# Optimization experiments

Hardware: AMD Instinct MI355X
Metric: run time of the kernel (lower is better)

## Reference

```python
import jax, jax.numpy as jnp
import numpy as np
from jax import lax

B, C, H, W = 4, 256, 64, 64
NH, DK, DV = 8, 32, 32
KER, PAD = 3, 1


def conv1x1(x, w, b=None):
    # x: [B,C,H,W], w: [O,C] (1x1 conv kernel), b: [O] or None
    y = jnp.einsum('bchw,oc->bohw', x, w)
    if b is not None:
        y = y + b[None, :, None, None]
    return y


def unfold(x, k, pad):
    # F.unfold equivalent: [B,C,H,W] -> [B, C*k*k, H, W] (channel-major patch order)
    return lax.conv_general_dilated_patches(x, (k, k), (1, 1), [(pad, pad), (pad, pad)])


def local_attention(q, k, v, kernel, pad, n_head):
    # per-head local windowed attention over a kernel x kernel neighborhood
    b, c, h, w = q.shape
    d = c // n_head
    kk = kernel * kernel
    qh = q.reshape(b, n_head, d, h, w)
    kpat = unfold(k, kernel, pad).reshape(b, n_head, d, kk, h, w)
    vpat = unfold(v, kernel, pad).reshape(b, n_head, d, kk, h, w)
    scale = 1.0 / np.sqrt(float(d)).astype(np.float32)
    logits = jnp.einsum('bhdxy,bhdkxy->bhkxy', qh, kpat) * scale
    attn = jax.nn.softmax(logits, axis=2)
    out = jnp.einsum('bhkxy,bhdkxy->bhdxy', attn, vpat)
    return out.reshape(b, c, h, w)


def layernorm2d(x, g, b, eps=1e-6):
    mu = jnp.mean(x, axis=1, keepdims=True)
    var = jnp.mean((x - mu) ** 2, axis=1, keepdims=True)
    return (x - mu) / jnp.sqrt(var + eps) * g[None, :, None, None] + b[None, :, None, None]


def batchnorm2d(x, g, b, eps=1e-5):
    mu = jnp.mean(x, axis=(0, 2, 3), keepdims=True)
    var = jnp.mean((x - mu) ** 2, axis=(0, 2, 3), keepdims=True)
    return (x - mu) / jnp.sqrt(var + eps) * g[None, :, None, None] + b[None, :, None, None]


def mha(xq, xkv, wq, wk, wv, wfc, g, bias, kernel, pad):
    residual = xq
    q = conv1x1(xq, wq)
    k = conv1x1(xkv, wk)
    v = conv1x1(xkv, wv)
    o = local_attention(q, k, v, kernel, pad, NH)
    o = conv1x1(o, wfc) + residual
    return layernorm2d(o, g, bias)


def ffn(x, w1, b1, w2, b2, g, bias):
    residual = x
    y = conv1x1(jax.nn.relu(conv1x1(x, w1, b1)), w2, b2)
    y = batchnorm2d(y, g, bias)
    return y + residual


def setup_inputs() -> dict:
    key = jax.random.key(0)
    ks = jax.random.split(key, 16)
    s = 0.05
    d = {
        'input1': jax.random.normal(ks[0], (B, C, H, W), jnp.float32),
        'input2': jax.random.normal(ks[1], (B, C, H, W), jnp.float32),
        'slf_wq': jax.random.normal(ks[2], (NH * DK, C), jnp.float32) * s,
        'slf_wk': jax.random.normal(ks[3], (NH * DK, C), jnp.float32) * s,
        'slf_wv': jax.random.normal(ks[4], (NH * DV, C), jnp.float32) * s,
        'slf_fc': jax.random.normal(ks[5], (C, NH * DV), jnp.float32) * s,
        'slf_g': jnp.ones((C,), jnp.float32),
        'slf_b': jnp.zeros((C,), jnp.float32),
        'crs_wq': jax.random.normal(ks[6], (NH * DK, C), jnp.float32) * s,
        'crs_wk': jax.random.normal(ks[7], (NH * DK, C), jnp.float32) * s,
        'crs_wv': jax.random.normal(ks[8], (NH * DV, C), jnp.float32) * s,
        'crs_fc': jax.random.normal(ks[9], (C, NH * DV), jnp.float32) * s,
        'crs_g': jnp.ones((C,), jnp.float32),
        'crs_b': jnp.zeros((C,), jnp.float32),
        'ffn_w1': jax.random.normal(ks[10], (C, C), jnp.float32) * s,
        'ffn_b1': jnp.zeros((C,), jnp.float32),
        'ffn_w2': jax.random.normal(ks[11], (C, C), jnp.float32) * s,
        'ffn_b2': jnp.zeros((C,), jnp.float32),
        'ffn_bn_g': jnp.ones((C,), jnp.float32),
        'ffn_bn_b': jnp.zeros((C,), jnp.float32),
        'kernel': KER,
        'pad': PAD,
    }
    return d


def reference(input1, input2, slf_wq, slf_wk, slf_wv, slf_fc, slf_g, slf_b,
              crs_wq, crs_wk, crs_wv, crs_fc, crs_g, crs_b,
              ffn_w1, ffn_b1, ffn_w2, ffn_b2, ffn_bn_g, ffn_bn_b, kernel, pad):
    slf1 = mha(input1, input1, slf_wq, slf_wk, slf_wv, slf_fc, slf_g, slf_b, kernel, pad)
    slf2 = mha(input2, input2, slf_wq, slf_wk, slf_wv, slf_fc, slf_g, slf_b, kernel, pad)
    crs1 = mha(slf1, slf2, crs_wq, crs_wk, crs_wv, crs_fc, crs_g, crs_b, kernel, pad)
    crs2 = mha(slf2, slf1, crs_wq, crs_wk, crs_wv, crs_fc, crs_g, crs_b, kernel, pad)
    out1 = ffn(crs1, ffn_w1, ffn_b1, ffn_w2, ffn_b2, ffn_bn_g, ffn_bn_b)
    out2 = ffn(crs2, ffn_w1, ffn_b1, ffn_w2, ffn_b2, ffn_bn_g, ffn_bn_b)
    return (out1, out2)
```

## Files before the change

kernel.cpp:

```cpp
#include <hip/hip_runtime.h>
#include <stdint.h>

using u16 = unsigned short;
typedef __bf16 bf16x8 __attribute__((ext_vector_type(8)));
typedef __bf16 bf16x2 __attribute__((ext_vector_type(2)));
typedef float f32x4 __attribute__((ext_vector_type(4)));

#define NPIX 16384
#define CDIM 256

__device__ __forceinline__ float b2f(u16 u) {
  union { unsigned i; float f; } c; c.i = ((unsigned)u) << 16; return c.f;
}
__device__ __forceinline__ u16 f2b(float x) {
  union { __bf16 h; u16 u; } c; c.h = (__bf16)x; return c.u;
}
__device__ __forceinline__ unsigned pack2(float a, float b) {
  union { bf16x2 v; unsigned u; } c; c.v[0] = (__bf16)a; c.v[1] = (__bf16)b; return c.u;
}
__device__ __forceinline__ void unpack8(uint4 w, float* f) {
  f[0] = b2f((u16)(w.x & 0xffffu)); f[1] = b2f((u16)(w.x >> 16));
  f[2] = b2f((u16)(w.y & 0xffffu)); f[3] = b2f((u16)(w.y >> 16));
  f[4] = b2f((u16)(w.z & 0xffffu)); f[5] = b2f((u16)(w.z >> 16));
  f[6] = b2f((u16)(w.w & 0xffffu)); f[7] = b2f((u16)(w.w >> 16));
}

__device__ __forceinline__ void async16(u16* l, const u16* g) {
  __builtin_amdgcn_global_load_lds((const __attribute__((address_space(1))) void*)g,
                                   (__attribute__((address_space(3))) void*)l, 16, 0, 0);
}

template <int NI, int NT>
__device__ __forceinline__ void stage_swz(u16* lds, const u16* src, int tid) {
#pragma unroll
  for (int i = 0; i < NI; ++i) {
    const int idx = i * NT + tid;
    const int row = idx >> 3;
    const int c8 = (idx & 7) ^ (row & 7);
    async16(lds + idx * 8, src + (size_t)row * 256 + c8 * 8);
  }
}

__global__ void prep(const float* __restrict__ x1, const float* __restrict__ x2,
                     u16* __restrict__ X1, u16* __restrict__ X2,
                     const float* s0, const float* s1, const float* s2,
                     const float* s3, const float* s4, const float* s5,
                     const float* s6, const float* s7, const float* s8,
                     const float* s9, u16* __restrict__ wdst,
                     float* __restrict__ stats) {
  const int t = threadIdx.x;
  const int yy = blockIdx.y;
  if (yy >= 32) {
    const int m = yy - 32;
    if (m == 0 && blockIdx.x == 0) {
      ((float4*)stats)[t] = float4{0.f, 0.f, 0.f, 0.f};
    }
    const float* s;
    switch (m) {
      case 0: s = s0; break; case 1: s = s1; break; case 2: s = s2; break;
      case 3: s = s3; break; case 4: s = s4; break; case 5: s = s5; break;
      case 6: s = s6; break; case 7: s = s7; break; case 8: s = s8; break;
      default: s = s9; break;
    }
    const int i = (blockIdx.x * 256 + t) * 4;
    float4 v = *(const float4*)(s + i);
    uint2 o;
    o.x = pack2(v.x, v.y);
    o.y = pack2(v.z, v.w);
    *(uint2*)(wdst + (size_t)m * 65536 + i) = o;
    return;
  }
  __shared__ u16 tile[64][65];
  const int z = yy >> 2;
  const float* x = (z < 4) ? x1 : x2;
  u16* X = (z < 4) ? X1 : X2;
  const int b = z & 3, c0 = (yy & 3) * 64, hw0 = blockIdx.x * 64;
  {
    const int hw_l = t & 63, cb = t >> 6;
#pragma unroll
    for (int i = 0; i < 16; ++i) {
      const int c_l = cb * 16 + i;
      tile[c_l][hw_l] = f2b(x[((size_t)(b * 256 + c0 + c_l)) * 4096 + hw0 + hw_l]);
    }
  }
  __syncthreads();
  {
    const int c_l = t & 63, hb = t >> 6;
#pragma unroll
    for (int i = 0; i < 16; ++i) {
      const int hw_l = hb * 16 + i;
      X[((size_t)(b * 4096 + hw0 + hw_l)) * 256 + c0 + c_l] = tile[c_l][hw_l];
    }
  }
}

struct PG { const u16* X[6]; const u16* W[3]; u16* D[6];
            const float* bias; float* st[2]; };

template <int NG, int HAS_BIAS, int RELU, int DO_STATS>
__global__ void gemm128(PG a) {
  __shared__ u16 As[2][8192];
  __shared__ u16 Bs[2][8192];
  const int tid = threadIdx.x;
  const int wave = tid >> 6, lane = tid & 63;
  const int p0 = blockIdx.x * 128;
  const int g = (NG == 3) ? (blockIdx.y >> 1) : 0;
  const int o0 = (NG == 3) ? ((blockIdx.y & 1) * 128) : (blockIdx.y * 128);
  const int z = blockIdx.z;
  const u16* X = a.X[z * NG + g];
  const u16* W = a.W[g];
  u16* D = a.D[z * NG + g];
  const int wr = wave & 1, wc = wave >> 1;
  const int l15 = lane & 15, l4 = lane >> 4;
  const int sw = l15 & 7;
  f32x4 acc[4][4] = {};

  const u16* Xp = X + (size_t)p0 * 256;
  const u16* Wp = W + (size_t)o0 * 256;
  stage_swz<4, 256>(As[0], Xp, tid);
  stage_swz<4, 256>(Bs[0], Wp, tid);
  __syncthreads();

  for (int kt = 0; kt < 4; ++kt) {
    const int cur = kt & 1;
    if (kt < 3) {
      stage_swz<4, 256>(As[cur ^ 1], Xp + (kt + 1) * 64, tid);
      stage_swz<4, 256>(Bs[cur ^ 1], Wp + (kt + 1) * 64, tid);
    }
    const u16* ab = As[cur];
    const u16* bb = Bs[cur];
#pragma unroll
    for (int kk = 0; kk < 2; ++kk) {
      const int cs = ((kk * 4 + l4) ^ sw) * 8;
      bf16x8 af[4], bfr[4];
#pragma unroll
      for (int mi = 0; mi < 4; ++mi)
        af[mi] = *(const bf16x8*)&ab[(wr * 64 + mi * 16 + l15) * 64 + cs];
#pragma unroll
      for (int ni = 0; ni < 4; ++ni)
        bfr[ni] = *(const bf16x8*)&bb[(wc * 64 + ni * 16 + l15) * 64 + cs];
#pragma unroll
      for (int mi = 0; mi < 4; ++mi)
#pragma unroll
        for (int ni = 0; ni < 4; ++ni)
          acc[mi][ni] = __builtin_amdgcn_mfma_f32_16x16x32_bf16(af[mi], bfr[ni],
                                                                acc[mi][ni], 0, 0, 0);
    }
    __syncthreads();
  }

#pragma unroll
  for (int ni = 0; ni < 4; ++ni) {
    const int o = o0 + wc * 64 + ni * 16 + l15;
    float bvv = 0.f;
    if (HAS_BIAS) bvv = a.bias[o];
    float s = 0.f, s2 = 0.f;
#pragma unroll
    for (int mi = 0; mi < 4; ++mi) {
#pragma unroll
      for (int r = 0; r < 4; ++r) {
        const int p = p0 + wr * 64 + mi * 16 + l4 * 4 + r;
        float v = acc[mi][ni][r] + bvv;
        if (RELU) v = fmaxf(v, 0.f);
        const u16 hv = f2b(v);
        D[(size_t)p * 256 + o] = hv;
        if (DO_STATS) { const float vr = b2f(hv); s += vr; s2 += vr * vr; }
      }
    }
    if (DO_STATS) {
      s += __shfl_xor(s, 16); s2 += __shfl_xor(s2, 16);
      s += __shfl_xor(s, 32); s2 += __shfl_xor(s2, 32);
      if (l4 == 0) {
        atomicAdd(&a.st[z][o], s);
        atomicAdd(&a.st[z][256 + o], s2);
      }
    }
  }
}

struct Pfc { const u16* X[2]; const u16* res[2]; u16* dst[2];
             const u16* W; const float* g; const float* b; };

__global__ __launch_bounds__(512) void gemm_fc_ln(Pfc a) {
  __shared__ u16 As[2][8192];
  __shared__ u16 Bs[2][16384];
  __shared__ float red[2][128][4];
  const int tid = threadIdx.x;
  const int wave = tid >> 6, lane = tid & 63;
  const int wr = wave & 1, wc = wave >> 1;
  const int l15 = lane & 15, l4 = lane >> 4;
  const int sw = l15 & 7;
  const int p0 = blockIdx.x * 128;
  const int z = blockIdx.y;
  const u16* X = a.X[z];
  const u16* res = a.res[z];
  u16* dst = a.dst[z];
  f32x4 acc[4][4] = {};

  const u16* Xp = X + (size_t)p0 * 256;
  stage_swz<2, 512>(As[0], Xp, tid);
  stage_swz<4, 512>(Bs[0], a.W, tid);
  __syncthreads();

  for (int kt = 0; kt < 4; ++kt) {
    const int cur = kt & 1;
    if (kt < 3) {
      stage_swz<2, 512>(As[cur ^ 1], Xp + (kt + 1) * 64, tid);
      stage_swz<4, 512>(Bs[cur ^ 1], a.W + (kt + 1) * 64, tid);
    }
    const u16* ab = As[cur];
    const u16* bb = Bs[cur];
#pragma unroll
    for (int kk = 0; kk < 2; ++kk) {
      const int cs = ((kk * 4 + l4) ^ sw) * 8;
      bf16x8 af[4], bfr[4];
#pragma unroll
      for (int mi = 0; mi < 4; ++mi)
        af[mi] = *(const bf16x8*)&ab[(wr * 64 + mi * 16 + l15) * 64 + cs];
#pragma unroll
      for (int ni = 0; ni < 4; ++ni)
        bfr[ni] = *(const bf16x8*)&bb[(wc * 64 + ni * 16 + l15) * 64 + cs];
#pragma unroll
      for (int mi = 0; mi < 4; ++mi)
#pragma unroll
        for (int ni = 0; ni < 4; ++ni)
          acc[mi][ni] = __builtin_amdgcn_mfma_f32_16x16x32_bf16(af[mi], bfr[ni],
                                                                acc[mi][ni], 0, 0, 0);
    }
    __syncthreads();
  }

#pragma unroll
  for (int mi = 0; mi < 4; ++mi) {
#pragma unroll
    for (int r = 0; r < 4; ++r) {
      const int pl = wr * 64 + mi * 16 + l4 * 4 + r;
      const int p = p0 + pl;
      float s = 0.f, s2 = 0.f;
#pragma unroll
      for (int ni = 0; ni < 4; ++ni) {
        const int o = wc * 64 + ni * 16 + l15;
        float vv = acc[mi][ni][r] + b2f(res[(size_t)p * 256 + o]);
        acc[mi][ni][r] = vv;
        s += vv; s2 += vv * vv;
      }
#pragma unroll
      for (int m = 1; m < 16; m <<= 1) {
        s += __shfl_xor(s, m); s2 += __shfl_xor(s2, m);
      }
      if (l15 == 0) { red[0][pl][wc] = s; red[1][pl][wc] = s2; }
    }
  }
  __syncthreads();

  float gv[4], bv[4];
#pragma unroll
  for (int ni = 0; ni < 4; ++ni) {
    const int o = wc * 64 + ni * 16 + l15;
    gv[ni] = a.g[o]; bv[ni] = a.b[o];
  }
#pragma unroll
  for (int mi = 0; mi < 4; ++mi) {
#pragma unroll
    for (int r = 0; r < 4; ++r) {
      const int pl = wr * 64 + mi * 16 + l4 * 4 + r;
      const float st = red[0][pl][0] + red[0][pl][1] + red[0][pl][2] + red[0][pl][3];
      const float s2t = red[1][pl][0] + red[1][pl][1] + red[1][pl][2] + red[1][pl][3];
      const float mu = st * (1.f / 256.f);
      const float var = s2t * (1.f / 256.f) - mu * mu;
      const float inv = rsqrtf(var + 1e-6f);
      const int p = p0 + pl;
#pragma unroll
      for (int ni = 0; ni < 4; ++ni) {
        const int o = wc * 64 + ni * 16 + l15;
        dst[(size_t)p * 256 + o] = f2b((acc[mi][ni][r] - mu) * inv * gv[ni] + bv[ni]);
      }
    }
  }
}

struct Pat { const u16* Q[2]; const u16* K[2]; const u16* V[2]; u16* O[2]; };

__global__ void attn_kernel(Pat a) {
  const int s = blockIdx.y;
  const u16* __restrict__ Q = a.Q[s];
  const u16* __restrict__ K = a.K[s];
  const u16* __restrict__ V = a.V[s];
  u16* O = a.O[s];
  const int t = blockIdx.x * 256 + threadIdx.x;
  const int p = t >> 3, h = t & 7;
  const int y = (p >> 6) & 63, x = p & 63;
  const size_t base = (size_t)p * 256 + h * 32;

  float q[32];
  {
    const uint4* qp = (const uint4*)(Q + base);
#pragma unroll
    for (int i = 0; i < 4; ++i) { uint4 w = qp[i]; unpack8(w, q + i * 8); }
  }
  float lg[9];
  float mx = -1e30f;
#pragma unroll
  for (int j = 0; j < 9; ++j) {
    const int dy = j / 3 - 1, dx = j % 3 - 1;
    const int ny = y + dy, nx = x + dx;
    float l = 0.f;
    if ((unsigned)ny < 64u && (unsigned)nx < 64u) {
      const uint4* kp = (const uint4*)(K + base + (ptrdiff_t)(dy * 64 + dx) * 256);
      float acc = 0.f;
#pragma unroll
      for (int i = 0; i < 4; ++i) {
        float kf[8]; unpack8(kp[i], kf);
#pragma unroll
        for (int d = 0; d < 8; ++d) acc += q[i * 8 + d] * kf[d];
      }
      l = acc * 0.17677669529663687f;
    }
    lg[j] = l;
    mx = fmaxf(mx, l);
  }
  float pr[9], den = 0.f;
#pragma unroll
  for (int j = 0; j < 9; ++j) { pr[j] = __expf(lg[j] - mx); den += pr[j]; }
  float out[32];
#pragma unroll
  for (int d = 0; d < 32; ++d) out[d] = 0.f;
#pragma unroll
  for (int j = 0; j < 9; ++j) {
    const int dy = j / 3 - 1, dx = j % 3 - 1;
    const int ny = y + dy, nx = x + dx;
    if ((unsigned)ny < 64u && (unsigned)nx < 64u) {
      const uint4* vp = (const uint4*)(V + base + (ptrdiff_t)(dy * 64 + dx) * 256);
      const float w = pr[j];
#pragma unroll
      for (int i = 0; i < 4; ++i) {
        float vf[8]; unpack8(vp[i], vf);
#pragma unroll
        for (int d = 0; d < 8; ++d) out[i * 8 + d] += w * vf[d];
      }
    }
  }
  const float inv = 1.f / den;
  uint4* op = (uint4*)(O + base);
#pragma unroll
  for (int i = 0; i < 4; ++i) {
    uint4 w;
    w.x = pack2(out[i * 8 + 0] * inv, out[i * 8 + 1] * inv);
    w.y = pack2(out[i * 8 + 2] * inv, out[i * 8 + 3] * inv);
    w.z = pack2(out[i * 8 + 4] * inv, out[i * 8 + 5] * inv);
    w.w = pack2(out[i * 8 + 6] * inv, out[i * 8 + 7] * inv);
    op[i] = w;
  }
}

struct Pbn { const u16* U[2]; const u16* res[2]; const float* st[2];
             float* out[2]; const float* g; const float* b; };

__global__ void bn_apply(Pbn a) {
  __shared__ float tile[64][65];
  const int t = threadIdx.x;
  const int s = blockIdx.z >> 2, b = blockIdx.z & 3;
  const u16* __restrict__ U = a.U[s];
  const u16* __restrict__ res = a.res[s];
  const float* st = a.st[s];
  float* out = a.out[s];
  const int c0 = blockIdx.y * 64, hw0 = blockIdx.x * 64;
  {
    const int c_l = t & 63, hb = t >> 6;
    const int c = c0 + c_l;
    const float mu = st[c] * (1.f / 16384.f);
    const float var = st[256 + c] * (1.f / 16384.f) - mu * mu;
    const float sc = rsqrtf(var + 1e-5f) * a.g[c];
    const float sh = a.b[c] - mu * sc;
#pragma unroll
    for (int i = 0; i < 16; ++i) {
      const int hw_l = hb * 16 + i;
      const size_t p = (size_t)b * 4096 + hw0 + hw_l;
      const float u = b2f(U[p * 256 + c]);
      const float r = b2f(res[p * 256 + c]);
      tile[hw_l][c_l] = u * sc + sh + r;
    }
  }
  __syncthreads();
  {
    const int hw_l = t & 63, cb2 = t >> 6;
#pragma unroll
    for (int i = 0; i < 16; ++i) {
      const int c_l = cb2 * 16 + i;
      out[((size_t)(b * 256 + c0 + c_l)) * 4096 + hw0 + hw_l] = tile[hw_l][c_l];
    }
  }
}

extern "C" void kernel_launch(void* const* d_in, const int* in_sizes, int n_in,
                              void* d_out, int out_size, void* d_ws, size_t ws_size,
                              hipStream_t stream) {
  const float* input1 = (const float*)d_in[0];
  const float* input2 = (const float*)d_in[1];
  const float* slf_wq = (const float*)d_in[2];
  const float* slf_wk = (const float*)d_in[3];
  const float* slf_wv = (const float*)d_in[4];
  const float* slf_fc = (const float*)d_in[5];
  const float* slf_g  = (const float*)d_in[6];
  const float* slf_b  = (const float*)d_in[7];
  const float* crs_wq = (const float*)d_in[8];
  const float* crs_wk = (const float*)d_in[9];
  const float* crs_wv = (const float*)d_in[10];
  const float* crs_fc = (const float*)d_in[11];
  const float* crs_g  = (const float*)d_in[12];
  const float* crs_b  = (const float*)d_in[13];
  const float* ffn_w1 = (const float*)d_in[14];
  const float* ffn_b1 = (const float*)d_in[15];
  const float* ffn_w2 = (const float*)d_in[16];
  const float* ffn_b2 = (const float*)d_in[17];
  const float* bn_g   = (const float*)d_in[18];
  const float* bn_b   = (const float*)d_in[19];

  float* out = (float*)d_out;
  u16* ws = (u16*)d_ws;
  const size_t TS = (size_t)NPIX * CDIM;
  u16* b[10];
  for (int i = 0; i < 10; ++i) b[i] = ws + (size_t)i * TS;
  u16* wb = ws + 10 * TS;
  u16 *Wsq = wb,             *Wsk = wb + 65536,     *Wsv = wb + 2 * 65536,
      *Wsf = wb + 3 * 65536, *Wcq = wb + 4 * 65536, *Wck = wb + 5 * 65536,
      *Wcv = wb + 6 * 65536, *Wcf = wb + 7 * 65536, *W1 = wb + 8 * 65536,
      *W2 = wb + 9 * 65536;
  float* stats = (float*)(wb + 10 * 65536);

  const dim3 tb(256);

  prep<<<dim3(64, 42), tb, 0, stream>>>(input1, input2, b[0], b[1],
                                        slf_wq, slf_wk, slf_wv, slf_fc,
                                        crs_wq, crs_wk, crs_wv, crs_fc,
                                        ffn_w1, ffn_w2, wb, stats);

  PG sa;
  sa.X[0] = b[0]; sa.X[1] = b[0]; sa.X[2] = b[0];
  sa.X[3] = b[1]; sa.X[4] = b[1]; sa.X[5] = b[1];
  sa.W[0] = Wsq; sa.W[1] = Wsk; sa.W[2] = Wsv;
  sa.D[0] = b[4]; sa.D[1] = b[5]; sa.D[2] = b[6];
  sa.D[3] = b[7]; sa.D[4] = b[8]; sa.D[5] = b[9];
  sa.bias = nullptr; sa.st[0] = nullptr; sa.st[1] = nullptr;
  gemm128<3, 0, 0, 0><<<dim3(NPIX / 128, 6, 2), tb, 0, stream>>>(sa);

  Pat aa;
  aa.Q[0] = b[4]; aa.Q[1] = b[7];
  aa.K[0] = b[5]; aa.K[1] = b[8];
  aa.V[0] = b[6]; aa.V[1] = b[9];
  aa.O[0] = b[4]; aa.O[1] = b[7];
  attn_kernel<<<dim3(NPIX * 8 / 256, 2), tb, 0, stream>>>(aa);

  Pfc f1;
  f1.X[0] = b[4]; f1.X[1] = b[7];
  f1.res[0] = b[0]; f1.res[1] = b[1];
  f1.dst[0] = b[2]; f1.dst[1] = b[3];
  f1.W = Wsf; f1.g = slf_g; f1.b = slf_b;
  gemm_fc_ln<<<dim3(NPIX / 128, 2), dim3(512), 0, stream>>>(f1);

  PG ca;
  ca.X[0] = b[2]; ca.X[1] = b[3]; ca.X[2] = b[3];
  ca.X[3] = b[3]; ca.X[4] = b[2]; ca.X[5] = b[2];
  ca.W[0] = Wcq; ca.W[1] = Wck; ca.W[2] = Wcv;
  ca.D[0] = b[4]; ca.D[1] = b[5]; ca.D[2] = b[6];
  ca.D[3] = b[7]; ca.D[4] = b[8]; ca.D[5] = b[9];
  ca.bias = nullptr; ca.st[0] = nullptr; ca.st[1] = nullptr;
  gemm128<3, 0, 0, 0><<<dim3(NPIX / 128, 6, 2), tb, 0, stream>>>(ca);
  attn_kernel<<<dim3(NPIX * 8 / 256, 2), tb, 0, stream>>>(aa);

  Pfc f2;
  f2.X[0] = b[4]; f2.X[1] = b[7];
  f2.res[0] = b[2]; f2.res[1] = b[3];
  f2.dst[0] = b[0]; f2.dst[1] = b[1];
  f2.W = Wcf; f2.g = crs_g; f2.b = crs_b;
  gemm_fc_ln<<<dim3(NPIX / 128, 2), dim3(512), 0, stream>>>(f2);

  PG g1;
  g1.X[0] = b[0]; g1.X[1] = b[1];
  g1.W[0] = W1;
  g1.D[0] = b[4]; g1.D[1] = b[7];
  g1.bias = ffn_b1; g1.st[0] = nullptr; g1.st[1] = nullptr;
  gemm128<1, 1, 1, 0><<<dim3(NPIX / 128, 2, 2), tb, 0, stream>>>(g1);

  PG g2;
  g2.X[0] = b[4]; g2.X[1] = b[7];
  g2.W[0] = W2;
  g2.D[0] = b[5]; g2.D[1] = b[8];
  g2.bias = ffn_b2; g2.st[0] = stats; g2.st[1] = stats + 512;
  gemm128<1, 1, 0, 1><<<dim3(NPIX / 128, 2, 2), tb, 0, stream>>>(g2);

  Pbn bn;
  bn.U[0] = b[5]; bn.U[1] = b[8];
  bn.res[0] = b[0]; bn.res[1] = b[1];
  bn.st[0] = stats; bn.st[1] = stats + 512;
  bn.out[0] = out; bn.out[1] = out + TS;
  bn.g = bn_g; bn.b = bn_b;
  bn_apply<<<dim3(64, 4, 8), tb, 0, stream>>>(bn);
}
```

Measured before the change: 301.6 us.

## Unroll GEMM K-loop with explicit waitcnt barriers and stage output through LDS

Both GEMM kernels have their K loop fully unrolled into an explicit double-buffered ping-pong. Each step uses vmcnt(0) plus an s_barrier, with sched_barrier fences so the compiler cannot hoist the async loads across the MFMA compute. The aim is better overlap of global-to-LDS loads with MFMA and less generic __syncthreads overhead. gemm128 also writes its bf16 output through a per-wave LDS slab so it can use coalesced 16-byte row stores instead of scattered 2-byte stores. The risk is a race between a wave's slab writes and other waves still reading the operand buffers, since there is a syncthreads before the slab, and more code size.

```diff
diff --git a/kernel.cpp b/kernel.cpp
--- a/kernel.cpp
+++ b/kernel.cpp
@@ -38,6 +38,33 @@
     const int row = idx >> 3;
     const int c8 = (idx & 7) ^ (row & 7);
     async16(lds + idx * 8, src + (size_t)row * 256 + c8 * 8);
+  }
+}
+
+__device__ __forceinline__ void wait_vm0_barrier() {
+  asm volatile("s_waitcnt vmcnt(0)" ::: "memory");
+  __builtin_amdgcn_s_barrier();
+}
+
+__device__ __forceinline__ void compute_tile(const u16* ab, const u16* bb,
+                                             f32x4 (&acc)[4][4], int wr, int wc,
+                                             int l15, int l4, int sw) {
+#pragma unroll
+  for (int kk = 0; kk < 2; ++kk) {
+    const int cs = ((kk * 4 + l4) ^ sw) * 8;
+    bf16x8 af[4], bfr[4];
+#pragma unroll
+    for (int mi = 0; mi < 4; ++mi)
+      af[mi] = *(const bf16x8*)&ab[(wr * 64 + mi * 16 + l15) * 64 + cs];
+#pragma unroll
+    for (int ni = 0; ni < 4; ++ni)
+      bfr[ni] = *(const bf16x8*)&bb[(wc * 64 + ni * 16 + l15) * 64 + cs];
+#pragma unroll
+    for (int mi = 0; mi < 4; ++mi)
+#pragma unroll
+      for (int ni = 0; ni < 4; ++ni)
+        acc[mi][ni] = __builtin_amdgcn_mfma_f32_16x16x32_bf16(af[mi], bfr[ni],
+                                                              acc[mi][ni], 0, 0, 0);
   }
 }
 
@@ -99,8 +126,8 @@
 
 template <int NG, int HAS_BIAS, int RELU, int DO_STATS>
 __global__ void gemm128(PG a) {
-  __shared__ u16 As[2][8192];
-  __shared__ u16 Bs[2][8192];
+  __shared__ u16 AsA[8192], AsB[8192];
+  __shared__ u16 BsA[8192], BsB[8192];
   const int tid = threadIdx.x;
   const int wave = tid >> 6, lane = tid & 63;
   const int p0 = blockIdx.x * 128;
@@ -117,38 +144,30 @@
 
   const u16* Xp = X + (size_t)p0 * 256;
   const u16* Wp = W + (size_t)o0 * 256;
-  stage_swz<4, 256>(As[0], Xp, tid);
-  stage_swz<4, 256>(Bs[0], Wp, tid);
+
+  stage_swz<4, 256>(AsA, Xp, tid);
+  stage_swz<4, 256>(BsA, Wp, tid);
+  wait_vm0_barrier();
+
+  stage_swz<4, 256>(AsB, Xp + 64, tid);
+  stage_swz<4, 256>(BsB, Wp + 64, tid);
+  __builtin_amdgcn_sched_barrier(0);
+  compute_tile(AsA, BsA, acc, wr, wc, l15, l4, sw);
+  wait_vm0_barrier();
+  stage_swz<4, 256>(AsA, Xp + 128, tid);
+  stage_swz<4, 256>(BsA, Wp + 128, tid);
+  __builtin_amdgcn_sched_barrier(0);
+  compute_tile(AsB, BsB, acc, wr, wc, l15, l4, sw);
+  wait_vm0_barrier();
+  stage_swz<4, 256>(AsB, Xp + 192, tid);
+  stage_swz<4, 256>(BsB, Wp + 192, tid);
+  __builtin_amdgcn_sched_barrier(0);
+  compute_tile(AsA, BsA, acc, wr, wc, l15, l4, sw);
+  wait_vm0_barrier();
+  compute_tile(AsB, BsB, acc, wr, wc, l15, l4, sw);
   __syncthreads();
 
-  for (int kt = 0; kt < 4; ++kt) {
-    const int cur = kt & 1;
-    if (kt < 3) {
-      stage_swz<4, 256>(As[cur ^ 1], Xp + (kt + 1) * 64, tid);
-      stage_swz<4, 256>(Bs[cur ^ 1], Wp + (kt + 1) * 64, tid);
-    }
-    const u16* ab = As[cur];
-    const u16* bb = Bs[cur];
-#pragma unroll
-    for (int kk = 0; kk < 2; ++kk) {
-      const int cs = ((kk * 4 + l4) ^ sw) * 8;
-      bf16x8 af[4], bfr[4];
-#pragma unroll
-      for (int mi = 0; mi < 4; ++mi)
-        af[mi] = *(const bf16x8*)&ab[(wr * 64 + mi * 16 + l15) * 64 + cs];
-#pragma unroll
-      for (int ni = 0; ni < 4; ++ni)
-        bfr[ni] = *(const bf16x8*)&bb[(wc * 64 + ni * 16 + l15) * 64 + cs];
-#pragma unroll
-      for (int mi = 0; mi < 4; ++mi)
-#pragma unroll
-        for (int ni = 0; ni < 4; ++ni)
-          acc[mi][ni] = __builtin_amdgcn_mfma_f32_16x16x32_bf16(af[mi], bfr[ni],
-                                                                acc[mi][ni], 0, 0, 0);
-    }
-    __syncthreads();
-  }
-
+  u16* slab = (wave == 0) ? AsA : (wave == 1) ? AsB : (wave == 2) ? BsA : BsB;
 #pragma unroll
   for (int ni = 0; ni < 4; ++ni) {
     const int o = o0 + wc * 64 + ni * 16 + l15;
@@ -159,11 +178,10 @@
     for (int mi = 0; mi < 4; ++mi) {
 #pragma unroll
       for (int r = 0; r < 4; ++r) {
-        const int p = p0 + wr * 64 + mi * 16 + l4 * 4 + r;
         float v = acc[mi][ni][r] + bvv;
         if (RELU) v = fmaxf(v, 0.f);
         const u16 hv = f2b(v);
-        D[(size_t)p * 256 + o] = hv;
+        slab[(mi * 16 + l4 * 4 + r) * 72 + ni * 16 + l15] = hv;
         if (DO_STATS) { const float vr = b2f(hv); s += vr; s2 += vr * vr; }
       }
     }
@@ -176,14 +194,22 @@
       }
     }
   }
+  asm volatile("s_waitcnt lgkmcnt(0)" ::: "memory");
+  __builtin_amdgcn_sched_barrier(0);
+  u16* Drow = D + (size_t)(p0 + wr * 64 + lane) * 256 + o0 + wc * 64;
+#pragma unroll
+  for (int c8 = 0; c8 < 8; ++c8) {
+    uint4 w = *(const uint4*)&slab[lane * 72 + c8 * 8];
+    *(uint4*)(Drow + c8 * 8) = w;
+  }
 }
 
 struct Pfc { const u16* X[2]; const u16* res[2]; u16* dst[2];
              const u16* W; const float* g; const float* b; };
 
 __global__ __launch_bounds__(512) void gemm_fc_ln(Pfc a) {
-  __shared__ u16 As[2][8192];
-  __shared__ u16 Bs[2][16384];
+  __shared__ u16 AsA[8192], AsB[8192];
+  __shared__ u16 BsA[16384], BsB[16384];
   __shared__ float red[2][128][4];
   const int tid = threadIdx.x;
   const int wave = tid >> 6, lane = tid & 63;
@@ -198,37 +224,27 @@
   f32x4 acc[4][4] = {};
 
   const u16* Xp = X + (size_t)p0 * 256;
-  stage_swz<2, 512>(As[0], Xp, tid);
-  stage_swz<4, 512>(Bs[0], a.W, tid);
-  __syncthreads();
-
-  for (int kt = 0; kt < 4; ++kt) {
-    const int cur = kt & 1;
-    if (kt < 3) {
-      stage_swz<2, 512>(As[cur ^ 1], Xp + (kt + 1) * 64, tid);
-      stage_swz<4, 512>(Bs[cur ^ 1], a.W + (kt + 1) * 64, tid);
-    }
-    const u16* ab = As[cur];
-    const u16* bb = Bs[cur];
-#pragma unroll
-    for (int kk = 0; kk < 2; ++kk) {
-      const int cs = ((kk * 4 + l4) ^ sw) * 8;
-      bf16x8 af[4], bfr[4];
-#pragma unroll
-      for (int mi = 0; mi < 4; ++mi)
-        af[mi] = *(const bf16x8*)&ab[(wr * 64 + mi * 16 + l15) * 64 + cs];
-#pragma unroll
-      for (int ni = 0; ni < 4; ++ni)
-        bfr[ni] = *(const bf16x8*)&bb[(wc * 64 + ni * 16 + l15) * 64 + cs];
-#pragma unroll
-      for (int mi = 0; mi < 4; ++mi)
-#pragma unroll
-        for (int ni = 0; ni < 4; ++ni)
-          acc[mi][ni] = __builtin_amdgcn_mfma_f32_16x16x32_bf16(af[mi], bfr[ni],
-                                                                acc[mi][ni], 0, 0, 0);
-    }
-    __syncthreads();
-  }
+
+  stage_swz<2, 512>(AsA, Xp, tid);
+  stage_swz<4, 512>(BsA, a.W, tid);
+  wait_vm0_barrier();
+
+  stage_swz<2, 512>(AsB, Xp + 64, tid);
+  stage_swz<4, 512>(BsB, a.W + 64, tid);
+  __builtin_amdgcn_sched_barrier(0);
+  compute_tile(AsA, BsA, acc, wr, wc, l15, l4, sw);
+  wait_vm0_barrier();
+  stage_swz<2, 512>(AsA, Xp + 128, tid);
+  stage_swz<4, 512>(BsA, a.W + 128, tid);
+  __builtin_amdgcn_sched_barrier(0);
+  compute_tile(AsB, BsB, acc, wr, wc, l15, l4, sw);
+  wait_vm0_barrier();
+  stage_swz<2, 512>(AsB, Xp + 192, tid);
+  stage_swz<4, 512>(BsB, a.W + 192, tid);
+  __builtin_amdgcn_sched_barrier(0);
+  compute_tile(AsA, BsA, acc, wr, wc, l15, l4, sw);
+  wait_vm0_barrier();
+  compute_tile(AsB, BsB, acc, wr, wc, l15, l4, sw);
 
 #pragma unroll
   for (int mi = 0; mi < 4; ++mi) {
```

After: 321.2 us. 6.5% more time.

## Fuse local attention into FC+LayerNorm GEMM and fuse both FFN GEMMs

Applied to the files above, without the earlier changes.

The standalone attention kernel is folded into the output-projection GEMM. Each block computes attention for its 128 pixels straight into swizzled LDS and then runs the FC GEMM plus LayerNorm from that tile, so the attention output never goes through global memory. The two FFN GEMMs are merged into one kernel that keeps the ReLU intermediate in LDS and feeds it to the second GEMM, which also gathers the batchnorm statistics. This removes global round-trips and kernel launches. The cost is much more LDS per block, lower occupancy, only 256 blocks per fused launch, and weight staging that is no longer double-buffered.

```diff
diff --git a/kernel.cpp b/kernel.cpp
--- a/kernel.cpp
+++ b/kernel.cpp
@@ -38,6 +38,28 @@
     const int row = idx >> 3;
     const int c8 = (idx & 7) ^ (row & 7);
     async16(lds + idx * 8, src + (size_t)row * 256 + c8 * 8);
+  }
+}
+
+__device__ __forceinline__ void compute_tile(const u16* ab, const u16* bb,
+                                             f32x4 (&acc)[4][4], int wr, int wc,
+                                             int l15, int l4, int sw) {
+#pragma unroll
+  for (int kk = 0; kk < 2; ++kk) {
+    const int cs = ((kk * 4 + l4) ^ sw) * 8;
+    bf16x8 af[4], bfr[4];
+#pragma unroll
+    for (int mi = 0; mi < 4; ++mi)
+      af[mi] = *(const bf16x8*)&ab[(wr * 64 + mi * 16 + l15) * 64 + cs];
+#pragma unroll
+    for (int ni = 0; ni < 4; ++ni)
+      bfr[ni] = *(const bf16x8*)&bb[(wc * 64 + ni * 16 + l15) * 64 + cs];
+#pragma unroll
+    for (int mi = 0; mi < 4; ++mi)
+#pragma unroll
+      for (int ni = 0; ni < 4; ++ni)
+        acc[mi][ni] = __builtin_amdgcn_mfma_f32_16x16x32_bf16(af[mi], bfr[ni],
+                                                              acc[mi][ni], 0, 0, 0);
   }
 }
 
@@ -94,22 +116,19 @@
   }
 }
 
-struct PG { const u16* X[6]; const u16* W[3]; u16* D[6];
-            const float* bias; float* st[2]; };
-
-template <int NG, int HAS_BIAS, int RELU, int DO_STATS>
-__global__ void gemm128(PG a) {
+struct PG { const u16* X[6]; const u16* W[3]; u16* D[6]; };
+
+__global__ void gemm_qkv(PG a) {
   __shared__ u16 As[2][8192];
   __shared__ u16 Bs[2][8192];
   const int tid = threadIdx.x;
   const int wave = tid >> 6, lane = tid & 63;
   const int p0 = blockIdx.x * 128;
-  const int g = (NG == 3) ? (blockIdx.y >> 1) : 0;
-  const int o0 = (NG == 3) ? ((blockIdx.y & 1) * 128) : (blockIdx.y * 128);
+  const int g = blockIdx.y >> 1, o0 = (blockIdx.y & 1) * 128;
   const int z = blockIdx.z;
-  const u16* X = a.X[z * NG + g];
+  const u16* X = a.X[z * 3 + g];
   const u16* W = a.W[g];
-  u16* D = a.D[z * NG + g];
+  u16* D = a.D[z * 3 + g];
   const int wr = wave & 1, wc = wave >> 1;
   const int l15 = lane & 15, l4 = lane >> 4;
   const int sw = l15 & 7;
@@ -127,63 +146,29 @@
       stage_swz<4, 256>(As[cur ^ 1], Xp + (kt + 1) * 64, tid);
       stage_swz<4, 256>(Bs[cur ^ 1], Wp + (kt + 1) * 64, tid);
     }
-    const u16* ab = As[cur];
-    const u16* bb = Bs[cur];
-#pragma unroll
-    for (int kk = 0; kk < 2; ++kk) {
-      const int cs = ((kk * 4 + l4) ^ sw) * 8;
-      bf16x8 af[4], bfr[4];
-#pragma unroll
-      for (int mi = 0; mi < 4; ++mi)
-        af[mi] = *(const bf16x8*)&ab[(wr * 64 + mi * 16 + l15) * 64 + cs];
-#pragma unroll
-      for (int ni = 0; ni < 4; ++ni)
-        bfr[ni] = *(const bf16x8*)&bb[(wc * 64 + ni * 16 + l15) * 64 + cs];
-#pragma unroll
-      for (int mi = 0; mi < 4; ++mi)
-#pragma unroll
-        for (int ni = 0; ni < 4; ++ni)
-          acc[mi][ni] = __builtin_amdgcn_mfma_f32_16x16x32_bf16(af[mi], bfr[ni],
-                                                                acc[mi][ni], 0, 0, 0);
-    }
-    __syncthreads();
-  }
-
+    compute_tile(As[cur], Bs[cur], acc, wr, wc, l15, l4, sw);
+    __syncthreads();
+  }
 #pragma unroll
   for (int ni = 0; ni < 4; ++ni) {
     const int o = o0 + wc * 64 + ni * 16 + l15;
-    float bvv = 0.f;
-    if (HAS_BIAS) bvv = a.bias[o];
-    float s = 0.f, s2 = 0.f;
-#pragma unroll
-    for (int mi = 0; mi < 4; ++mi) {
+#pragma unroll
+    for (int mi = 0; mi < 4; ++mi)
 #pragma unroll
       for (int r = 0; r < 4; ++r) {
         const int p = p0 + wr * 64 + mi * 16 + l4 * 4 + r;
-        float v = acc[mi][ni][r] + bvv;
-        if (RELU) v = fmaxf(v, 0.f);
-        const u16 hv = f2b(v);
-        D[(size_t)p * 256 + o] = hv;
-        if (DO_STATS) { const float vr = b2f(hv); s += vr; s2 += vr * vr; }
-      }
-    }
-    if (DO_STATS) {
-      s += __shfl_xor(s, 16); s2 += __shfl_xor(s2, 16);
-      s += __shfl_xor(s, 32); s2 += __shfl_xor(s2, 32);
-      if (l4 == 0) {
-        atomicAdd(&a.st[z][o], s);
-        atomicAdd(&a.st[z][256 + o], s2);
-      }
-    }
-  }
-}
-
-struct Pfc { const u16* X[2]; const u16* res[2]; u16* dst[2];
+        D[(size_t)p * 256 + o] = f2b(acc[mi][ni][r]);
+      }
+  }
+}
+
+struct Paf { const u16* Q[2]; const u16* K[2]; const u16* V[2];
+             const u16* res[2]; u16* dst[2];
              const u16* W; const float* g; const float* b; };
 
-__global__ __launch_bounds__(512) void gemm_fc_ln(Pfc a) {
-  __shared__ u16 As[2][8192];
-  __shared__ u16 Bs[2][16384];
+__global__ __launch_bounds__(512) void attn_fc_ln(Paf a) {
+  __shared__ u16 A4[4 * 8192];
+  __shared__ u16 Bs[16384];
   __shared__ float red[2][128][4];
   const int tid = threadIdx.x;
   const int wave = tid >> 6, lane = tid & 63;
@@ -192,42 +177,90 @@
   const int sw = l15 & 7;
   const int p0 = blockIdx.x * 128;
   const int z = blockIdx.y;
-  const u16* X = a.X[z];
-  const u16* res = a.res[z];
+  const u16* __restrict__ Q = a.Q[z];
+  const u16* __restrict__ K = a.K[z];
+  const u16* __restrict__ V = a.V[z];
+  const u16* __restrict__ res = a.res[z];
   u16* dst = a.dst[z];
+
+  stage_swz<4, 512>(Bs, a.W, tid);
+
+#pragma unroll
+  for (int u = 0; u < 2; ++u) {
+    const int pp = u * 512 + tid;
+    const int p_l = pp >> 3, h = pp & 7;
+    const int p = p0 + p_l;
+    const int y = (p >> 6) & 63, x = p & 63;
+    const size_t base = (size_t)p * 256 + h * 32;
+
+    float q[32];
+    {
+      const uint4* qp = (const uint4*)(Q + base);
+#pragma unroll
+      for (int i = 0; i < 4; ++i) { uint4 w = qp[i]; unpack8(w, q + i * 8); }
+    }
+    float lg[9];
+    float mx = -1e30f;
+#pragma unroll
+    for (int j = 0; j < 9; ++j) {
+      const int dy = j / 3 - 1, dx = j % 3 - 1;
+      const int ny = y + dy, nx = x + dx;
+      float l = 0.f;
+      if ((unsigned)ny < 64u && (unsigned)nx < 64u) {
+        const uint4* kp = (const uint4*)(K + base + (ptrdiff_t)(dy * 64 + dx) * 256);
+        float acq = 0.f;
+#pragma unroll
+        for (int i = 0; i < 4; ++i) {
+          float kf[8]; unpack8(kp[i], kf);
+#pragma unroll
+          for (int d = 0; d < 8; ++d) acq += q[i * 8 + d] * kf[d];
+        }
+        l = acq * 0.17677669529663687f;
+      }
+      lg[j] = l;
+      mx = fmaxf(mx, l);
+    }
+    float pr[9], den = 0.f;
+#pragma unroll
+    for (int j = 0; j < 9; ++j) { pr[j] = __expf(lg[j] - mx); den += pr[j]; }
+    float out[32];
+#pragma unroll
+    for (int d = 0; d < 32; ++d) out[d] = 0.f;
+#pragma unroll
+    for (int j = 0; j < 9; ++j) {
+      const int dy = j / 3 - 1, dx = j % 3 - 1;
+      const int ny = y + dy, nx = x + dx;
+      if ((unsigned)ny < 64u && (unsigned)nx < 64u) {
+        const uint4* vp = (const uint4*)(V + base + (ptrdiff_t)(dy * 64 + dx) * 256);
+        const float w = pr[j];
+#pragma unroll
+        for (int i = 0; i < 4; ++i) {
+          float vf[8]; unpack8(vp[i], vf);
+#pragma unroll
+          for (int d = 0; d < 8; ++d) out[i * 8 + d] += w * vf[d];
+        }
+      }
+    }
+    const float inv = 1.f / den;
+    u16* dl = A4 + (h >> 1) * 8192 + p_l * 64;
+#pragma unroll
+    for (int i = 0; i < 4; ++i) {
+      uint4 w;
+      w.x = pack2(out[i * 8 + 0] * inv, out[i * 8 + 1] * inv);
+      w.y = pack2(out[i * 8 + 2] * inv, out[i * 8 + 3] * inv);
+      w.z = pack2(out[i * 8 + 4] * inv, out[i * 8 + 5] * inv);
+      w.w = pack2(out[i * 8 + 6] * inv, out[i * 8 + 7] * inv);
+      const int c8 = (h & 1) * 4 + i;
+      *(uint4*)&dl[(c8 ^ (p_l & 7)) * 8] = w;
+    }
+  }
+
   f32x4 acc[4][4] = {};
-
-  const u16* Xp = X + (size_t)p0 * 256;
-  stage_swz<2, 512>(As[0], Xp, tid);
-  stage_swz<4, 512>(Bs[0], a.W, tid);
-  __syncthreads();
-
   for (int kt = 0; kt < 4; ++kt) {
-    const int cur = kt & 1;
-    if (kt < 3) {
-      stage_swz<2, 512>(As[cur ^ 1], Xp + (kt + 1) * 64, tid);
-      stage_swz<4, 512>(Bs[cur ^ 1], a.W + (kt + 1) * 64, tid);
-    }
-    const u16* ab = As[cur];
-    const u16* bb = Bs[cur];
-#pragma unroll
-    for (int kk = 0; kk < 2; ++kk) {
-      const int cs = ((kk * 4 + l4) ^ sw) * 8;
-      bf16x8 af[4], bfr[4];
-#pragma unroll
-      for (int mi = 0; mi < 4; ++mi)
-        af[mi] = *(const bf16x8*)&ab[(wr * 64 + mi * 16 + l15) * 64 + cs];
-#pragma unroll
-      for (int ni = 0; ni < 4; ++ni)
-        bfr[ni] = *(const bf16x8*)&bb[(wc * 64 + ni * 16 + l15) * 64 + cs];
-#pragma unroll
-      for (int mi = 0; mi < 4; ++mi)
-#pragma unroll
-        for (int ni = 0; ni < 4; ++ni)
-          acc[mi][ni] = __builtin_amdgcn_mfma_f32_16x16x32_bf16(af[mi], bfr[ni],
-                                                                acc[mi][ni], 0, 0, 0);
-    }
-    __syncthreads();
+    __syncthreads();
+    compute_tile(A4 + kt * 8192, Bs, acc, wr, wc, l15, l4, sw);
+    __syncthreads();
+    if (kt < 3) stage_swz<4, 512>(Bs, a.W + (kt + 1) * 64, tid);
   }
 
 #pragma unroll
@@ -279,77 +312,79 @@
   }
 }
 
-struct Pat { const u16* Q[2]; const u16* K[2]; const u16* V[2]; u16* O[2]; };
-
-__global__ void attn_kernel(Pat a) {
-  const int s = blockIdx.y;
-  const u16* __restrict__ Q = a.Q[s];
-  const u16* __restrict__ K = a.K[s];
-  const u16* __restrict__ V = a.V[s];
-  u16* O = a.O[s];
-  const int t = blockIdx.x * 256 + threadIdx.x;
-  const int p = t >> 3, h = t & 7;
-  const int y = (p >> 6) & 63, x = p & 63;
-  const size_t base = (size_t)p * 256 + h * 32;
-
-  float q[32];
+struct Pff { const u16* X[2]; u16* U[2]; float* st[2];
+             const u16* W1; const float* b1; const u16* W2; const float* b2; };
+
+__global__ __launch_bounds__(512) void ffn_fused(Pff a) {
+  __shared__ u16 mid[4 * 8192];
+  __shared__ u16 As[8192];
+  __shared__ u16 Bs[16384];
+  const int tid = threadIdx.x;
+  const int wave = tid >> 6, lane = tid & 63;
+  const int wr = wave & 1, wc = wave >> 1;
+  const int l15 = lane & 15, l4 = lane >> 4;
+  const int sw = l15 & 7;
+  const int p0 = blockIdx.x * 128;
+  const int z = blockIdx.y;
+  const u16* X = a.X[z];
+  u16* U = a.U[z];
+  float* st = a.st[z];
+  const u16* Xp = X + (size_t)p0 * 256;
+
+  f32x4 acc1[4][4] = {};
+  for (int kt = 0; kt < 4; ++kt) {
+    stage_swz<2, 512>(As, Xp + kt * 64, tid);
+    stage_swz<4, 512>(Bs, a.W1 + kt * 64, tid);
+    __syncthreads();
+    compute_tile(As, Bs, acc1, wr, wc, l15, l4, sw);
+    __syncthreads();
+  }
   {
-    const uint4* qp = (const uint4*)(Q + base);
-#pragma unroll
-    for (int i = 0; i < 4; ++i) { uint4 w = qp[i]; unpack8(w, q + i * 8); }
-  }
-  float lg[9];
-  float mx = -1e30f;
-#pragma unroll
-  for (int j = 0; j < 9; ++j) {
-    const int dy = j / 3 - 1, dx = j % 3 - 1;
-    const int ny = y + dy, nx = x + dx;
-    float l = 0.f;
-    if ((unsigned)ny < 64u && (unsigned)nx < 64u) {
-      const uint4* kp = (const uint4*)(K + base + (ptrdiff_t)(dy * 64 + dx) * 256);
-      float acc = 0.f;
-#pragma unroll
-      for (int i = 0; i < 4; ++i) {
-        float kf[8]; unpack8(kp[i], kf);
-#pragma unroll
-        for (int d = 0; d < 8; ++d) acc += q[i * 8 + d] * kf[d];
-      }
-      l = acc * 0.17677669529663687f;
-    }
-    lg[j] = l;
-    mx = fmaxf(mx, l);
-  }
-  float pr[9], den = 0.f;
-#pragma unroll
-  for (int j = 0; j < 9; ++j) { pr[j] = __expf(lg[j] - mx); den += pr[j]; }
-  float out[32];
-#pragma unroll
-  for (int d = 0; d < 32; ++d) out[d] = 0.f;
-#pragma unroll
-  for (int j = 0; j < 9; ++j) {
-    const int dy = j / 3 - 1, dx = j % 3 - 1;
-    const int ny = y + dy, nx = x + dx;
-    if ((unsigned)ny < 64u && (unsigned)nx < 64u) {
-      const uint4* vp = (const uint4*)(V + base + (ptrdiff_t)(dy * 64 + dx) * 256);
-      const float w = pr[j];
-#pragma unroll
-      for (int i = 0; i < 4; ++i) {
-        float vf[8]; unpack8(vp[i], vf);
-#pragma unroll
-        for (int d = 0; d < 8; ++d) out[i * 8 + d] += w * vf[d];
-      }
-    }
-  }
-  const float inv = 1.f / den;
-  uint4* op = (uint4*)(O + base);
-#pragma unroll
-  for (int i = 0; i < 4; ++i) {
-    uint4 w;
-    w.x = pack2(out[i * 8 + 0] * inv, out[i * 8 + 1] * inv);
-    w.y = pack2(out[i * 8 + 2] * inv, out[i * 8 + 3] * inv);
-    w.z = pack2(out[i * 8 + 4] * inv, out[i * 8 + 5] * inv);
-    w.w = pack2(out[i * 8 + 6] * inv, out[i * 8 + 7] * inv);
-    op[i] = w;
+    float bvv[4];
+#pragma unroll
+    for (int ni = 0; ni < 4; ++ni) bvv[ni] = a.b1[wc * 64 + ni * 16 + l15];
+    u16* ml = mid + wc * 8192;
+#pragma unroll
+    for (int mi = 0; mi < 4; ++mi) {
+#pragma unroll
+      for (int r = 0; r < 4; ++r) {
+        const int pl = wr * 64 + mi * 16 + l4 * 4 + r;
+#pragma unroll
+        for (int ni = 0; ni < 4; ++ni) {
+          const int col = ni * 16 + l15;
+          const int c8 = col >> 3;
+          const u16 hv = f2b(fmaxf(acc1[mi][ni][r] + bvv[ni], 0.f));
+          ml[pl * 64 + ((c8 ^ (pl & 7)) * 8) + (col & 7)] = hv;
+        }
+      }
+    }
+  }
+
+  f32x4 acc2[4][4] = {};
+  for (int kt = 0; kt < 4; ++kt) {
+    __syncthreads();
+    stage_swz<4, 512>(Bs, a.W2 + kt * 64, tid);
+    __syncthreads();
+    compute_tile(mid + kt * 8192, Bs, acc2, wr, wc, l15, l4, sw);
+  }
+#pragma unroll
+  for (int ni = 0; ni < 4; ++ni) {
+    const int o = wc * 64 + ni * 16 + l15;
+    const float bvv = a.b2[o];
+    float s = 0.f, s2 = 0.f;
+#pragma unroll
+    for (int mi = 0; mi < 4; ++mi) {
+#pragma unroll
+      for (int r = 0; r < 4; ++r) {
+        const int p = p0 + wr * 64 + mi * 16 + l4 * 4 + r;
+        const u16 hv = f2b(acc2[mi][ni][r] + bvv);
+        U[(size_t)p * 256 + o] = hv;
+        const float vr = b2f(hv); s += vr; s2 += vr * vr;
+      }
+    }
+    s += __shfl_xor(s, 16); s2 += __shfl_xor(s2, 16);
+    s += __shfl_xor(s, 32); s2 += __shfl_xor(s2, 32);
+    if (l4 == 0) { atomicAdd(&st[o], s); atomicAdd(&st[256 + o], s2); }
   }
 }
 
@@ -441,22 +476,15 @@
   sa.W[0] = Wsq; sa.W[1] = Wsk; sa.W[2] = Wsv;
   sa.D[0] = b[4]; sa.D[1] = b[5]; sa.D[2] = b[6];
   sa.D[3] = b[7]; sa.D[4] = b[8]; sa.D[5] = b[9];
-  sa.bias = nullptr; sa.st[0] = nullptr; sa.st[1] = nullptr;
-  gemm128<3, 0, 0, 0><<<dim3(NPIX / 128, 6, 2), tb, 0, stream>>>(sa);
-
-  Pat aa;
-  aa.Q[0] = b[4]; aa.Q[1] = b[7];
-  aa.K[0] = b[5]; aa.K[1] = b[8];
-  aa.V[0] = b[6]; aa.V[1] = b[9];
-  aa.O[0] = b[4]; aa.O[1] = b[7];
-  attn_kernel<<<dim3(NPIX * 8 / 256, 2), tb, 0, stream>>>(aa);
-
-  Pfc f1;
-  f1.X[0] = b[4]; f1.X[1] = b[7];
+  gemm_qkv<<<dim3(NPIX / 128, 6, 2), tb, 0, stream>>>(sa);
+
+  Paf f1;
+  f1.Q[0] = b[4]; f1.K[0] = b[5]; f1.V[0] = b[6];
+  f1.Q[1] = b[7]; f1.K[1] = b[8]; f1.V[1] = b[9];
   f1.res[0] = b[0]; f1.res[1] = b[1];
   f1.dst[0] = b[2]; f1.dst[1] = b[3];
   f1.W = Wsf; f1.g = slf_g; f1.b = slf_b;
-  gemm_fc_ln<<<dim3(NPIX / 128, 2), dim3(512), 0, stream>>>(f1);
+  attn_fc_ln<<<dim3(NPIX / 128, 2), dim3(512), 0, stream>>>(f1);
 
   PG ca;
   ca.X[0] = b[2]; ca.X[1] = b[3]; ca.X[2] = b[3];
@@ -464,33 +492,25 @@
   ca.W[0] = Wcq; ca.W[1] = Wck; ca.W[2] = Wcv;
   ca.D[0] = b[4]; ca.D[1] = b[5]; ca.D[2] = b[6];
   ca.D[3] = b[7]; ca.D[4] = b[8]; ca.D[5] = b[9];
-  ca.bias = nullptr; ca.st[0] = nullptr; ca.st[1] = nullptr;
-  gemm128<3, 0, 0, 0><<<dim3(NPIX / 128, 6, 2), tb, 0, stream>>>(ca);
-  attn_kernel<<<dim3(NPIX * 8 / 256, 2), tb, 0, stream>>>(aa);
-
-  Pfc f2;
-  f2.X[0] = b[4]; f2.X[1] = b[7];
+  gemm_qkv<<<dim3(NPIX / 128, 6, 2), tb, 0, stream>>>(ca);
+
+  Paf f2;
+  f2.Q[0] = b[4]; f2.K[0] = b[5]; f2.V[0] = b[6];
+  f2.Q[1] = b[7]; f2.K[1] = b[8]; f2.V[1] = b[9];
   f2.res[0] = b[2]; f2.res[1] = b[3];
   f2.dst[0] = b[0]; f2.dst[1] = b[1];
   f2.W = Wcf; f2.g = crs_g; f2.b = crs_b;
-  gemm_fc_ln<<<dim3(NPIX / 128, 2), dim3(512), 0, stream>>>(f2);
-
-  PG g1;
-  g1.X[0] = b[0]; g1.X[1] = b[1];
-  g1.W[0] = W1;
-  g1.D[0] = b[4]; g1.D[1] = b[7];
-  g1.bias = ffn_b1; g1.st[0] = nullptr; g1.st[1] = nullptr;
-  gemm128<1, 1, 1, 0><<<dim3(NPIX / 128, 2, 2), tb, 0, stream>>>(g1);
-
-  PG g2;
-  g2.X[0] = b[4]; g2.X[1] = b[7];
-  g2.W[0] = W2;
-  g2.D[0] = b[5]; g2.D[1] = b[8];
-  g2.bias = ffn_b2; g2.st[0] = stats; g2.st[1] = stats + 512;
-  gemm128<1, 1, 0, 1><<<dim3(NPIX / 128, 2, 2), tb, 0, stream>>>(g2);
+  attn_fc_ln<<<dim3(NPIX / 128, 2), dim3(512), 0, stream>>>(f2);
+
+  Pff ff;
+  ff.X[0] = b[0]; ff.X[1] = b[1];
+  ff.U[0] = b[4]; ff.U[1] = b[7];
+  ff.st[0] = stats; ff.st[1] = stats + 512;
+  ff.W1 = W1; ff.b1 = ffn_b1; ff.W2 = W2; ff.b2 = ffn_b2;
+  ffn_fused<<<dim3(NPIX / 128, 2), dim3(512), 0, stream>>>(ff);
 
   Pbn bn;
-  bn.U[0] = b[5]; bn.U[1] = b[8];
+  bn.U[0] = b[4]; bn.U[1] = b[7];
   bn.res[0] = b[0]; bn.res[1] = b[1];
   bn.st[0] = stats; bn.st[1] = stats + 512;
   bn.out[0] = out; bn.out[1] = out + TS;
```

Result: faster. 278.3 us (-7.7%).
